# Performance work log

Hardware: AMD Instinct MI355X
Metric: run time of the kernel (lower is better)

The kernel has to match this reference:

```python
import jax, jax.numpy as jnp
import numpy as np
import math

L, D, H, HD, F, G, V, P = 15, 512, 64, 8, 2048, 128, 7, 49
B, N = 4, 256


def setup_inputs() -> dict:
    key = jax.random.key(0)
    ks = jax.random.split(key, 24)
    nrm = lambda k, shape, s=0.02: (jax.random.normal(k, shape) * s).astype(jnp.float32)
    inp = {}
    inp["atom_types"] = jax.random.randint(ks[0], (B, N), 0, V)
    inp["coords"] = jax.random.normal(ks[1], (B, N, 3)) * 3.0
    inp["pair_types"] = jax.random.randint(ks[2], (B, N, N), 0, P)
    inp["mask"] = jnp.ones((B, N), dtype=bool)
    # embeddings / pair encoding params
    inp["atom_emb"] = nrm(ks[3], (V, D), 1.0).at[0].set(0.0)  # padding_idx=0
    inp["gaussian_mu"] = jax.random.normal(ks[4], (G,))
    inp["gaussian_sigma"] = jnp.ones((G,)) * 0.1
    inp["pair_a"] = jax.random.normal(ks[5], (P,)) * 0.01
    inp["pair_b"] = jax.random.normal(ks[6], (P,)) * 0.01
    inp["pl_w"] = nrm(ks[7], (G,))
    inp["pl_b"] = jnp.zeros(())
    # stacked per-layer params (leading dim L for lax.scan)
    inp["ln1_g"] = jnp.ones((L, D)); inp["ln1_b"] = jnp.zeros((L, D))
    inp["qkv_w"] = nrm(ks[8], (L, 3 * D, D)); inp["qkv_b"] = jnp.zeros((L, 3 * D))
    inp["pp_w"] = nrm(ks[9], (L, H), 0.1); inp["pp_b"] = jnp.zeros((L, H))
    inp["out_w"] = nrm(ks[10], (L, D, D)); inp["out_b"] = jnp.zeros((L, D))
    inp["ln2_g"] = jnp.ones((L, D)); inp["ln2_b"] = jnp.zeros((L, D))
    inp["ffn_w1"] = nrm(ks[11], (L, F, D)); inp["ffn_b1"] = jnp.zeros((L, F))
    inp["ffn_w2"] = nrm(ks[12], (L, D, F)); inp["ffn_b2"] = jnp.zeros((L, D))
    # SE3 head scalar affines (Linear(1,1) twice) and energy head
    inp["se3_uw"] = jnp.array(0.5); inp["se3_ub"] = jnp.array(0.01)
    inp["se3_ww"] = jnp.array(0.5); inp["se3_wb"] = jnp.array(0.01)
    inp["en_w"] = nrm(ks[13], (D,)); inp["en_b"] = jnp.zeros(())
    return inp


def _layernorm(x, g, b):
    m = x.mean(-1, keepdims=True)
    v = ((x - m) ** 2).mean(-1, keepdims=True)
    return (x - m) / jnp.sqrt(v + 1e-5) * g + b


def reference(atom_types, coords, pair_types, mask,
              atom_emb, gaussian_mu, gaussian_sigma, pair_a, pair_b, pl_w, pl_b,
              ln1_g, ln1_b, qkv_w, qkv_b, pp_w, pp_b, out_w, out_b,
              ln2_g, ln2_b, ffn_w1, ffn_b1, ffn_w2, ffn_b2,
              se3_uw, se3_ub, se3_ww, se3_wb, en_w, en_b):
    b_, n_ = atom_types.shape
    h = atom_emb[atom_types]  # [B,N,D]

    delta = coords[:, :, None, :] - coords[:, None, :, :]  # [B,N,N,3]
    d2 = (delta ** 2).sum(-1)
    dist = jnp.sqrt(jnp.maximum(d2, 1e-12))  # safe norm (grad-safe at 0)
    dist = jnp.where(mask[:, :, None], dist, 0.0)
    da = (pair_a[pair_types] * dist + pair_b[pair_types])[..., None]  # [B,N,N,1]
    gt = jnp.exp(-(da - gaussian_mu) ** 2) / (2.0 * gaussian_sigma ** 2)
    gt = gt / (gaussian_sigma * math.sqrt(2.0 * math.pi))
    gt = gt * mask[:, :, None, None]  # [B,N,N,G]
    pair_repr = gt @ pl_w + pl_b  # [B,N,N]
    pair_mask = mask[:, :, None] & mask[:, None, :]
    pair_repr = pair_repr * pair_mask

    scale = 1.0 / math.sqrt(HD)
    row_mask = mask[:, None, :, None]  # masks query rows, per original code

    def layer(hc, p):
        (l1g, l1b, qw, qb, ppw, ppb, ow, ob, l2g, l2b, w1, b1, w2, b2) = p
        x = _layernorm(hc, l1g, l1b)
        qkv = (x @ qw.T + qb).reshape(b_, n_, 3, H, HD)
        q, k, v = qkv[:, :, 0], qkv[:, :, 1], qkv[:, :, 2]
        scores = jnp.einsum('bnhd,bmhd->bhnm', q, k) * scale
        bias = pair_repr[..., None] * ppw + ppb  # [B,N,N,H]
        scores = scores + bias.transpose(0, 3, 1, 2)
        scores = jnp.where(row_mask, scores, -1e9)
        probs = jax.nn.softmax(scores, axis=-1)
        probs = jnp.where(jnp.isnan(probs), 0.0, probs)
        attn = jnp.einsum('bhnm,bmhd->bnhd', probs, v).reshape(b_, n_, D)
        hc = hc + attn @ ow.T + ob
        x2 = _layernorm(hc, l2g, l2b)
        ffn = jax.nn.gelu(x2 @ w1.T + b1, approximate=False) @ w2.T + b2
        return hc + ffn, None

    h, _ = jax.lax.scan(layer, h, (ln1_g, ln1_b, qkv_w, qkv_b, pp_w, pp_b,
                                   out_w, out_b, ln2_g, ln2_b,
                                   ffn_w1, ffn_b1, ffn_w2, ffn_b2))

    # --- SE3 equivariant head ---
    c = jax.nn.relu(pair_repr)[..., None]  # [B,N,N,1]
    c = c * se3_uw + se3_ub
    c = c * se3_ww + se3_wb
    c = c * mask[:, :, None, None]
    update = (delta * c).sum(axis=2)  # [B,N,3]
    num_valid = mask.sum(-1).astype(coords.dtype)[:, None, None] + 1e-6
    pred_coords = coords + update / num_valid

    cls = h[:, 0, :]
    pred_energy = cls @ en_w + en_b  # [B]
    return pred_coords, pred_energy


if __name__ == '__main__':
    out = reference(**setup_inputs())
    print(out[0].shape, out[1].shape)
```

## Files before the change

kernel.cpp:

```cpp
#include <hip/hip_runtime.h>
#include <hip/hip_bf16.h>
#include <math.h>

#define LAY 15
#define DIM 512
#define NH 64
#define HD 8
#define FF 2048
#define NG 128
#define BATCH 4
#define NTOK 256
#define PSTRIDE 524288

typedef __attribute__((ext_vector_type(8))) short short8;
typedef __attribute__((ext_vector_type(4))) short short4v;
typedef __attribute__((ext_vector_type(2))) short short2v;
typedef __attribute__((ext_vector_type(8))) __bf16 bf16x8;
typedef __attribute__((ext_vector_type(4))) float f32x4;

__device__ inline short f2bs(float f) {
  __bf16 b = (__bf16)f;
  return __builtin_bit_cast(short, b);
}

__global__ __launch_bounds__(256) void embed_kernel(
    const int* __restrict__ types, const float* __restrict__ emb,
    float* __restrict__ h)
{
  int idx = blockIdx.x * 256 + threadIdx.x;
  int token = idx >> 9;
  int d = idx & 511;
  h[idx] = emb[types[token] * DIM + d];
}

__global__ __launch_bounds__(256) void cvt2_kernel(
    const float* __restrict__ qkvw, const float* __restrict__ outw,
    const float* __restrict__ w1, const float* __restrict__ w2,
    short* __restrict__ dst, int basePair)
{
  size_t i = ((size_t)basePair + blockIdx.x * 256 + threadIdx.x) * 2;
  const float* src; size_t off;
  if (i < 1474560)      { src = qkvw; off = i; }
  else if (i < 1966080) { src = outw; off = i - 1474560; }
  else if (i < 3932160) { src = w1;   off = i - 1966080; }
  else                  { src = w2;   off = i - 3932160; }
  const float4* sp = (const float4*)(src + off * 8);
  float4 a = sp[0], b = sp[1], c = sp[2], d = sp[3];
  bf16x8 v0, v1;
  v0[0] = (__bf16)a.x; v0[1] = (__bf16)a.y; v0[2] = (__bf16)a.z; v0[3] = (__bf16)a.w;
  v0[4] = (__bf16)b.x; v0[5] = (__bf16)b.y; v0[6] = (__bf16)b.z; v0[7] = (__bf16)b.w;
  v1[0] = (__bf16)c.x; v1[1] = (__bf16)c.y; v1[2] = (__bf16)c.z; v1[3] = (__bf16)c.w;
  v1[4] = (__bf16)d.x; v1[5] = (__bf16)d.y; v1[6] = (__bf16)d.z; v1[7] = (__bf16)d.w;
  *(short8*)(dst + i * 8) = __builtin_bit_cast(short8, v0);
  *(short8*)(dst + i * 8 + 8) = __builtin_bit_cast(short8, v1);
}

__global__ __launch_bounds__(256) void pair_kernel(
    const int* __restrict__ pair_types, const float* __restrict__ coords,
    const float* __restrict__ mu, const float* __restrict__ sigma,
    const float* __restrict__ pa, const float* __restrict__ pb,
    const float* __restrict__ plw, const float* __restrict__ plb,
    const float* __restrict__ uw, const float* __restrict__ ub,
    const float* __restrict__ ww, const float* __restrict__ wb,
    float* __restrict__ pair_repr, float* __restrict__ out)
{
  __shared__ float smu[NG], sw[NG];
  __shared__ float sm[4][3];
  int tid = threadIdx.x;
  if (tid < NG) {
    float sg = sigma[tid];
    smu[tid] = mu[tid];
    sw[tid] = plw[tid] / (2.0f * sg * sg * sg * 2.5066282746310002f);
  }
  __syncthreads();
  int bi = blockIdx.x;
  int b = bi >> 8;
  int j = tid;
  int idx = bi * 256 + j;
  const float* ci = coords + bi * 3;
  const float* cj = coords + (b * NTOK + j) * 3;
  float dx = ci[0] - cj[0], dy = ci[1] - cj[1], dz = ci[2] - cj[2];
  float d2 = dx * dx + dy * dy + dz * dz;
  float dist = sqrtf(fmaxf(d2, 1e-12f));
  int pt = pair_types[idx];
  float da = pa[pt] * dist + pb[pt];
  float acc = 0.0f;
#pragma unroll 8
  for (int g = 0; g < NG; ++g) {
    float t = da - smu[g];
    acc += __expf(-t * t) * sw[g];
  }
  float pr = acc + plb[0];
  pair_repr[idx] = pr;

  float c = fmaxf(pr, 0.0f);
  c = c * uw[0] + ub[0];
  c = c * ww[0] + wb[0];
  float sx = dx * c, sy = dy * c, sz = dz * c;
#pragma unroll
  for (int o = 32; o > 0; o >>= 1) {
    sx += __shfl_xor(sx, o);
    sy += __shfl_xor(sy, o);
    sz += __shfl_xor(sz, o);
  }
  if ((j & 63) == 0) {
    sm[j >> 6][0] = sx; sm[j >> 6][1] = sy; sm[j >> 6][2] = sz;
  }
  __syncthreads();
  if (j < 3) {
    float u = sm[0][j] + sm[1][j] + sm[2][j] + sm[3][j];
    out[bi * 3 + j] = coords[bi * 3 + j] + u * (1.0f / (256.0f + 1e-6f));
  }
}

__global__ __launch_bounds__(256) void pairT_kernel(
    const float* __restrict__ pr, float* __restrict__ prT)
{
  __shared__ float tile[32][33];
  int b = blockIdx.z;
  int i0 = blockIdx.y * 32, j0 = blockIdx.x * 32;
  int tx = threadIdx.x & 31, ty = threadIdx.x >> 5;
#pragma unroll
  for (int r = 0; r < 4; ++r)
    tile[ty + r * 8][tx] = pr[((size_t)(b * NTOK + i0 + ty + r * 8)) * NTOK + j0 + tx];
  __syncthreads();
#pragma unroll
  for (int r = 0; r < 4; ++r)
    prT[((size_t)(b * NTOK + j0 + ty + r * 8)) * NTOK + i0 + tx] = tile[tx][ty + r * 8];
}

__global__ __launch_bounds__(256) void ln_kernel(
    const float* __restrict__ h, const float* __restrict__ g,
    const float* __restrict__ beta, short* __restrict__ x)
{
  int t = blockIdx.x;
  int tid = threadIdx.x;
  float2 v = *(const float2*)&h[(size_t)t * DIM + tid * 2];
  __shared__ float sm[4];
  float s = v.x + v.y;
#pragma unroll
  for (int o = 32; o > 0; o >>= 1) s += __shfl_xor(s, o);
  if ((tid & 63) == 0) sm[tid >> 6] = s;
  __syncthreads();
  float mean = (sm[0] + sm[1] + sm[2] + sm[3]) * (1.0f / 512.0f);
  float d0 = v.x - mean, d1 = v.y - mean;
  float ss = d0 * d0 + d1 * d1;
#pragma unroll
  for (int o = 32; o > 0; o >>= 1) ss += __shfl_xor(ss, o);
  __syncthreads();
  if ((tid & 63) == 0) sm[tid >> 6] = ss;
  __syncthreads();
  float var = (sm[0] + sm[1] + sm[2] + sm[3]) * (1.0f / 512.0f);
  float rstd = rsqrtf(var + 1e-5f);
  float2 gg = *(const float2*)&g[tid * 2];
  float2 bb = *(const float2*)&beta[tid * 2];
  short2v o2;
  o2[0] = f2bs(d0 * rstd * gg.x + bb.x);
  o2[1] = f2bs(d1 * rstd * gg.y + bb.y);
  *(short2v*)&x[(size_t)t * DIM + tid * 2] = o2;
}

__global__ __launch_bounds__(256) void ln_res_kernel(
    float* __restrict__ h, const float* __restrict__ part, int kparts,
    const float* __restrict__ g, const float* __restrict__ beta,
    short* __restrict__ x)
{
  int t = blockIdx.x;
  int tid = threadIdx.x;
  size_t base = (size_t)t * DIM + tid * 2;
  float2 v = *(const float2*)&h[base];
  for (int z = 0; z < kparts; ++z) {
    float2 pz = *(const float2*)&part[(size_t)z * PSTRIDE + base];
    v.x += pz.x; v.y += pz.y;
  }
  *(float2*)&h[base] = v;
  __shared__ float sm[4];
  float s = v.x + v.y;
#pragma unroll
  for (int o = 32; o > 0; o >>= 1) s += __shfl_xor(s, o);
  if ((tid & 63) == 0) sm[tid >> 6] = s;
  __syncthreads();
  float mean = (sm[0] + sm[1] + sm[2] + sm[3]) * (1.0f / 512.0f);
  float d0 = v.x - mean, d1 = v.y - mean;
  float ss = d0 * d0 + d1 * d1;
#pragma unroll
  for (int o = 32; o > 0; o >>= 1) ss += __shfl_xor(ss, o);
  __syncthreads();
  if ((tid & 63) == 0) sm[tid >> 6] = ss;
  __syncthreads();
  float var = (sm[0] + sm[1] + sm[2] + sm[3]) * (1.0f / 512.0f);
  float rstd = rsqrtf(var + 1e-5f);
  float2 gg = *(const float2*)&g[tid * 2];
  float2 bb = *(const float2*)&beta[tid * 2];
  short2v o2;
  o2[0] = f2bs(d0 * rstd * gg.x + bb.x);
  o2[1] = f2bs(d1 * rstd * gg.y + bb.y);
  *(short2v*)&x[base] = o2;
}

template <int MODE>
__global__ __launch_bounds__(128) void mm3(
    const short* __restrict__ A, const short* __restrict__ W,
    const float* __restrict__ bias, float* __restrict__ Cf,
    short* __restrict__ Cb, int N, int K, int kparts)
{
  __shared__ short As[2][2048];
  __shared__ short Bs[2][8192];
  int tid = threadIdx.x;
  int lane = tid & 63, wv = tid >> 6;
  int fr = lane & 15, fq = lane >> 4;
  int m0 = blockIdx.y * 32, n0 = blockIdx.x * 128;
  int Ksub = K / kparts;
  int kbeg = blockIdx.z * Ksub, kend = kbeg + Ksub;

  int arow[2], acol[2], brow[8], bcol[8];
#pragma unroll
  for (int r = 0; r < 2; ++r) {
    int id = r * 128 + tid;
    arow[r] = id >> 3;
    acol[r] = (id & 7) ^ (arow[r] & 7);
  }
#pragma unroll
  for (int r = 0; r < 8; ++r) {
    int id = r * 128 + tid;
    brow[r] = id >> 3;
    bcol[r] = (id & 7) ^ (brow[r] & 7);
  }

  auto stage = [&](int p, int k0) {
#pragma unroll
    for (int r = 0; r < 2; ++r) {
      const short* ga = &A[(size_t)(m0 + arow[r]) * K + k0 + acol[r] * 8];
      __builtin_amdgcn_global_load_lds(
          (const __attribute__((address_space(1))) void*)ga,
          (__attribute__((address_space(3))) void*)&As[p][(r * 128 + wv * 64) * 8],
          16, 0, 0);
    }
#pragma unroll
    for (int r = 0; r < 8; ++r) {
      const short* gw = &W[(size_t)(n0 + brow[r]) * K + k0 + bcol[r] * 8];
      __builtin_amdgcn_global_load_lds(
          (const __attribute__((address_space(1))) void*)gw,
          (__attribute__((address_space(3))) void*)&Bs[p][(r * 128 + wv * 64) * 8],
          16, 0, 0);
    }
  };

  f32x4 acc[2][4];
#pragma unroll
  for (int i = 0; i < 2; ++i)
#pragma unroll
    for (int j = 0; j < 4; ++j) acc[i][j] = (f32x4){0.f, 0.f, 0.f, 0.f};

  int aslot[2][2], bslot[2][4];
#pragma unroll
  for (int s = 0; s < 2; ++s) {
    int c = s * 4 + fq;
#pragma unroll
    for (int i = 0; i < 2; ++i) {
      int m = i * 16 + fr;
      aslot[s][i] = m * 8 + (c ^ (m & 7));
    }
#pragma unroll
    for (int j = 0; j < 4; ++j) {
      int n = wv * 64 + j * 16 + fr;
      bslot[s][j] = n * 8 + (c ^ (n & 7));
    }
  }

  stage(0, kbeg);
  __syncthreads();
  int p = 0;
  for (int k0 = kbeg; k0 < kend; k0 += 64) {
    if (k0 + 64 < kend) stage(p ^ 1, k0 + 64);
    short8 af[2][2], bf_[2][4];
#pragma unroll
    for (int s = 0; s < 2; ++s) {
#pragma unroll
      for (int i = 0; i < 2; ++i)
        af[s][i] = *(const short8*)&As[p][aslot[s][i] * 8];
#pragma unroll
      for (int j = 0; j < 4; ++j)
        bf_[s][j] = *(const short8*)&Bs[p][bslot[s][j] * 8];
    }
#pragma unroll
    for (int s = 0; s < 2; ++s)
#pragma unroll
      for (int i = 0; i < 2; ++i)
#pragma unroll
        for (int j = 0; j < 4; ++j)
          acc[i][j] = __builtin_amdgcn_mfma_f32_16x16x32_bf16(
              af[s][i], bf_[s][j], acc[i][j], 0, 0, 0);
    __syncthreads();
    p ^= 1;
  }

#pragma unroll
  for (int i = 0; i < 2; ++i) {
#pragma unroll
    for (int j = 0; j < 4; ++j) {
      int col = n0 + wv * 64 + j * 16 + fr;
      float bcol = bias[col];
#pragma unroll
      for (int rr = 0; rr < 4; ++rr) {
        int row = m0 + i * 16 + fq * 4 + rr;
        size_t idx = (size_t)row * N + col;
        float v = acc[i][j][rr];
        if (MODE == 2) {
          v += bcol;
          Cb[idx] = f2bs(0.5f * v * (1.0f + erff(v * 0.70710678118654752f)));
        } else if (MODE == 3) {
          Cb[idx] = f2bs(v + bcol);
        } else {
          if (blockIdx.z == 0) v += bcol;
          Cf[(size_t)blockIdx.z * PSTRIDE + idx] = v;
        }
      }
    }
  }
}

__global__ __launch_bounds__(128) void attn_mfma(
    const short* __restrict__ qkv, const float* __restrict__ prT,
    const float* __restrict__ ppw, const float* __restrict__ ppb,
    short* __restrict__ attn)
{
  __shared__ alignas(16) short Kl[256 * 8];
  __shared__ alignas(16) short Ql[128 * 8];
  __shared__ alignas(16) short VT[8 * 264];
  __shared__ alignas(16) short P[2 * 16 * 264];
  __shared__ alignas(16) float linv[32];
  int h = blockIdx.x, b = blockIdx.y;
  int qbase = blockIdx.z * 128;
  int tid = threadIdx.x;

#pragma unroll
  for (int r0 = 0; r0 < 2; ++r0) {
    int r = tid + r0 * 128;
    short8 kv = *(const short8*)&qkv[(size_t)(b * NTOK + r) * 1536 + 512 + h * 8];
    *(short8*)&Kl[r * 8] = kv;
    short8 vv = *(const short8*)&qkv[(size_t)(b * NTOK + r) * 1536 + 1024 + h * 8];
#pragma unroll
    for (int d = 0; d < 8; ++d) VT[d * 264 + r] = vv[d];
  }
  {
    short8 qv = *(const short8*)&qkv[(size_t)(b * NTOK + qbase + tid) * 1536 + h * 8];
    *(short8*)&Ql[tid * 8] = qv;
  }
  __syncthreads();

  int lane = tid & 63, w = tid >> 6;
  int fr = lane & 15, quad = lane >> 4;
  float pw = ppw[h], pbb = ppb[h];
  const float scale = 0.35355339059327373f;
  short8 zero8 = {0, 0, 0, 0, 0, 0, 0, 0};

  short8 vfrag[8];
#pragma unroll
  for (int kc = 0; kc < 8; ++kc)
    vfrag[kc] = (fr < 8) ? *(const short8*)&VT[fr * 264 + kc * 32 + quad * 8]
                         : zero8;

  short* Pw = &P[w * 16 * 264];
  float* lw = &linv[w * 16];

  for (int qt = 0; qt < 4; ++qt) {
    int qloc = w * 64 + qt * 16;
    int qg = qbase + qloc + fr;
    const float* prp = &prT[(size_t)b * 65536 + qg];
    float prv[16][4];
#pragma unroll
    for (int t = 0; t < 16; ++t)
#pragma unroll
      for (int r = 0; r < 4; ++r)
        prv[t][r] = prp[(size_t)(t * 16 + quad * 4 + r) * NTOK];

    short8 qf = zero8;
    if (quad == 0) qf = *(const short8*)&Ql[(qloc + fr) * 8];
    f32x4 sacc[16];
#pragma unroll
    for (int t = 0; t < 16; ++t) {
      short8 kf = zero8;
      if (quad == 0) kf = *(const short8*)&Kl[(t * 16 + fr) * 8];
      sacc[t] = __builtin_amdgcn_mfma_f32_16x16x32_bf16(
          kf, qf, (f32x4){0.f, 0.f, 0.f, 0.f}, 0, 0, 0);
    }

    float l = 0.f;
#pragma unroll
    for (int t = 0; t < 16; ++t) {
      short4v pk;
#pragma unroll
      for (int r = 0; r < 4; ++r) {
        float s = sacc[t][r] * scale + prv[t][r] * pw + pbb;
        float p = __expf(s);
        l += p;
        pk[r] = f2bs(p);
      }
      *(short4v*)&Pw[fr * 264 + t * 16 + quad * 4] = pk;
    }
    l += __shfl_xor(l, 16);
    l += __shfl_xor(l, 32);
    if (lane < 16) lw[fr] = 1.0f / l;

    f32x4 oacc = (f32x4){0.f, 0.f, 0.f, 0.f};
#pragma unroll
    for (int kc = 0; kc < 8; ++kc) {
      short8 pf = *(const short8*)&Pw[fr * 264 + kc * 32 + quad * 8];
      oacc = __builtin_amdgcn_mfma_f32_16x16x32_bf16(pf, vfrag[kc], oacc, 0, 0, 0);
    }
    if (fr < 8) {
      f32x4 li = *(f32x4*)&lw[quad * 4];
#pragma unroll
      for (int r = 0; r < 4; ++r) {
        int q = qbase + qloc + quad * 4 + r;
        attn[(size_t)(b * NTOK + q) * DIM + h * 8 + fr] = f2bs(oacc[r] * li[r]);
      }
    }
  }
}

__global__ __launch_bounds__(256) void energy_kernel(
    const float* __restrict__ h, const float* __restrict__ part,
    const float* __restrict__ enw, const float* __restrict__ enb,
    float* __restrict__ out)
{
  int b = blockIdx.x;
  int tid = threadIdx.x;
  size_t base = (size_t)(b * NTOK) * DIM;
  float x0 = h[base + tid], x1 = h[base + tid + 256];
#pragma unroll
  for (int z = 0; z < 4; ++z) {
    x0 += part[(size_t)z * PSTRIDE + base + tid];
    x1 += part[(size_t)z * PSTRIDE + base + tid + 256];
  }
  float s = x0 * enw[tid] + x1 * enw[tid + 256];
  __shared__ float sm[4];
#pragma unroll
  for (int o = 32; o > 0; o >>= 1) s += __shfl_xor(s, o);
  if ((tid & 63) == 0) sm[tid >> 6] = s;
  __syncthreads();
  if (tid == 0) out[BATCH * NTOK * 3 + b] = sm[0] + sm[1] + sm[2] + sm[3] + enb[0];
}

extern "C" void kernel_launch(void* const* d_in, const int* in_sizes, int n_in,
                              void* d_out, int out_size, void* d_ws, size_t ws_size,
                              hipStream_t stream)
{
  const int*   atom_types = (const int*)d_in[0];
  const float* coords     = (const float*)d_in[1];
  const int*   pair_types = (const int*)d_in[2];
  const float* atom_emb = (const float*)d_in[4];
  const float* gmu  = (const float*)d_in[5];
  const float* gsig = (const float*)d_in[6];
  const float* pa   = (const float*)d_in[7];
  const float* pb   = (const float*)d_in[8];
  const float* plw  = (const float*)d_in[9];
  const float* plb  = (const float*)d_in[10];
  const float* ln1g = (const float*)d_in[11];
  const float* ln1b = (const float*)d_in[12];
  const float* qkvw = (const float*)d_in[13];
  const float* qkvb = (const float*)d_in[14];
  const float* ppw  = (const float*)d_in[15];
  const float* ppb  = (const float*)d_in[16];
  const float* outw = (const float*)d_in[17];
  const float* outb = (const float*)d_in[18];
  const float* ln2g = (const float*)d_in[19];
  const float* ln2b = (const float*)d_in[20];
  const float* w1   = (const float*)d_in[21];
  const float* b1   = (const float*)d_in[22];
  const float* w2   = (const float*)d_in[23];
  const float* b2   = (const float*)d_in[24];
  const float* uw   = (const float*)d_in[25];
  const float* ub   = (const float*)d_in[26];
  const float* sww  = (const float*)d_in[27];
  const float* swb  = (const float*)d_in[28];
  const float* enw  = (const float*)d_in[29];
  const float* enb  = (const float*)d_in[30];

  float* out = (float*)d_out;
  float* ws  = (float*)d_ws;
  float* pair_repr = ws;
  float* prT  = pair_repr + 262144;
  float* h    = prT + 262144;
  float* part = h + 524288;
  short* qkv_bf  = (short*)(part + 4 * 524288);
  short* x_bf    = qkv_bf + 1572864;
  short* attn_bf = x_bf + 524288;
  short* ffn1_bf = attn_bf + 524288;
  short* qkvw_bf = ffn1_bf + 2097152;
  short* outw_bf = qkvw_bf + 11796480;
  short* w1_bf   = outw_bf + 3932160;
  short* w2_bf   = w1_bf + 15728640;

  cvt2_kernel<<<11520, 256, 0, stream>>>(qkvw, outw, w1, w2, qkvw_bf, 0);

  embed_kernel<<<2048, 256, 0, stream>>>(atom_types, atom_emb, h);
  pair_kernel<<<1024, 256, 0, stream>>>(pair_types, coords, gmu, gsig, pa, pb,
                                        plw, plb, uw, ub, sww, swb,
                                        pair_repr, out);
  pairT_kernel<<<dim3(8, 8, 4), 256, 0, stream>>>(pair_repr, prT);

  for (int l = 0; l < LAY; ++l) {
    if (l == 0)
      ln_kernel<<<1024, 256, 0, stream>>>(h, ln1g, ln1b, x_bf);
    else
      ln_res_kernel<<<1024, 256, 0, stream>>>(h, part, 4,
                                              ln1g + l * DIM, ln1b + l * DIM, x_bf);
    mm3<3><<<dim3(12, 32, 1), 128, 0, stream>>>(
        x_bf, qkvw_bf + (size_t)l * 1536 * DIM, qkvb + l * 1536, nullptr, qkv_bf,
        1536, DIM, 1);
    attn_mfma<<<dim3(NH, BATCH, 2), 128, 0, stream>>>(
        qkv_bf, prT, ppw + l * NH, ppb + l * NH, attn_bf);
    mm3<4><<<dim3(4, 32, 2), 128, 0, stream>>>(
        attn_bf, outw_bf + (size_t)l * DIM * DIM, outb + l * DIM, part, nullptr,
        DIM, DIM, 2);
    ln_res_kernel<<<1024, 256, 0, stream>>>(h, part, 2,
                                            ln2g + l * DIM, ln2b + l * DIM, x_bf);
    mm3<2><<<dim3(16, 32, 1), 128, 0, stream>>>(
        x_bf, w1_bf + (size_t)l * FF * DIM, b1 + l * FF, nullptr, ffn1_bf,
        FF, DIM, 1);
    mm3<4><<<dim3(4, 32, 4), 128, 0, stream>>>(
        ffn1_bf, w2_bf + (size_t)l * DIM * FF, b2 + l * DIM, part, nullptr,
        DIM, FF, 4);
  }
  energy_kernel<<<BATCH, 256, 0, stream>>>(h, part, enw, enb, out);
}
```

Baseline: 1.246 ms.

## Shrink GEMM tiles to single-wave 32x32 with triple-buffered async loads

Each GEMM block becomes one wave computing a 32x32 tile instead of two waves computing 32x128. The K loop is fully unrolled with a 3-stage LDS ring, using explicit vmcnt waits instead of __syncthreads so prefetches overlap the MFMAs. This quadruples the block count to fill more CUs, at the cost of more redundant A-tile loads and less reuse per block. The weight conversion kernel is also simplified to convert four floats per thread.

```diff
diff --git a/kernel.cpp b/kernel.cpp
--- a/kernel.cpp
+++ b/kernel.cpp
@@ -33,26 +33,21 @@
   h[idx] = emb[types[token] * DIM + d];
 }
 
-__global__ __launch_bounds__(256) void cvt2_kernel(
+__global__ __launch_bounds__(256) void cvt_kernel(
     const float* __restrict__ qkvw, const float* __restrict__ outw,
     const float* __restrict__ w1, const float* __restrict__ w2,
-    short* __restrict__ dst, int basePair)
-{
-  size_t i = ((size_t)basePair + blockIdx.x * 256 + threadIdx.x) * 2;
-  const float* src; size_t off;
-  if (i < 1474560)      { src = qkvw; off = i; }
-  else if (i < 1966080) { src = outw; off = i - 1474560; }
-  else if (i < 3932160) { src = w1;   off = i - 1966080; }
-  else                  { src = w2;   off = i - 3932160; }
-  const float4* sp = (const float4*)(src + off * 8);
-  float4 a = sp[0], b = sp[1], c = sp[2], d = sp[3];
-  bf16x8 v0, v1;
-  v0[0] = (__bf16)a.x; v0[1] = (__bf16)a.y; v0[2] = (__bf16)a.z; v0[3] = (__bf16)a.w;
-  v0[4] = (__bf16)b.x; v0[5] = (__bf16)b.y; v0[6] = (__bf16)b.z; v0[7] = (__bf16)b.w;
-  v1[0] = (__bf16)c.x; v1[1] = (__bf16)c.y; v1[2] = (__bf16)c.z; v1[3] = (__bf16)c.w;
-  v1[4] = (__bf16)d.x; v1[5] = (__bf16)d.y; v1[6] = (__bf16)d.z; v1[7] = (__bf16)d.w;
-  *(short8*)(dst + i * 8) = __builtin_bit_cast(short8, v0);
-  *(short8*)(dst + i * 8 + 8) = __builtin_bit_cast(short8, v1);
+    short* __restrict__ dst)
+{
+  int i = blockIdx.x * 256 + threadIdx.x;
+  const float* src; int off;
+  if (i < 2949120)      { src = qkvw; off = i; }
+  else if (i < 3932160) { src = outw; off = i - 2949120; }
+  else if (i < 7864320) { src = w1;   off = i - 3932160; }
+  else                  { src = w2;   off = i - 7864320; }
+  float4 f = ((const float4*)src)[off];
+  short4v o;
+  o[0] = f2bs(f.x); o[1] = f2bs(f.y); o[2] = f2bs(f.z); o[3] = f2bs(f.w);
+  *(short4v*)(dst + (size_t)i * 4) = o;
 }
 
 __global__ __launch_bounds__(256) void pair_kernel(
@@ -198,61 +193,51 @@
   *(short2v*)&x[base] = o2;
 }
 
-template <int MODE>
-__global__ __launch_bounds__(128) void mm3(
+template <int MODE, int TSTEPS>
+__global__ __launch_bounds__(64) void mm3(
     const short* __restrict__ A, const short* __restrict__ W,
     const float* __restrict__ bias, float* __restrict__ Cf,
-    short* __restrict__ Cb, int N, int K, int kparts)
-{
-  __shared__ short As[2][2048];
-  __shared__ short Bs[2][8192];
+    short* __restrict__ Cb, int N, int K)
+{
+  __shared__ alignas(16) short As[3][2048];
+  __shared__ alignas(16) short Bs[3][2048];
   int tid = threadIdx.x;
-  int lane = tid & 63, wv = tid >> 6;
-  int fr = lane & 15, fq = lane >> 4;
-  int m0 = blockIdx.y * 32, n0 = blockIdx.x * 128;
-  int Ksub = K / kparts;
-  int kbeg = blockIdx.z * Ksub, kend = kbeg + Ksub;
-
-  int arow[2], acol[2], brow[8], bcol[8];
-#pragma unroll
-  for (int r = 0; r < 2; ++r) {
-    int id = r * 128 + tid;
-    arow[r] = id >> 3;
-    acol[r] = (id & 7) ^ (arow[r] & 7);
-  }
-#pragma unroll
-  for (int r = 0; r < 8; ++r) {
-    int id = r * 128 + tid;
-    brow[r] = id >> 3;
-    bcol[r] = (id & 7) ^ (brow[r] & 7);
-  }
+  int fr = tid & 15, fq = (tid >> 4) & 3;
+  int m0 = blockIdx.y * 32, n0 = blockIdx.x * 32;
+  int kbeg = blockIdx.z * (TSTEPS * 64);
 
   auto stage = [&](int p, int k0) {
 #pragma unroll
-    for (int r = 0; r < 2; ++r) {
-      const short* ga = &A[(size_t)(m0 + arow[r]) * K + k0 + acol[r] * 8];
+    for (int r = 0; r < 4; ++r) {
+      int id = r * 64 + tid;
+      int row = id >> 3;
+      int col = (id & 7) ^ (row & 7);
+      const short* ga = &A[(size_t)(m0 + row) * K + k0 + col * 8];
       __builtin_amdgcn_global_load_lds(
           (const __attribute__((address_space(1))) void*)ga,
-          (__attribute__((address_space(3))) void*)&As[p][(r * 128 + wv * 64) * 8],
+          (__attribute__((address_space(3))) void*)&As[p][r * 512],
           16, 0, 0);
     }
 #pragma unroll
-    for (int r = 0; r < 8; ++r) {
-      const short* gw = &W[(size_t)(n0 + brow[r]) * K + k0 + bcol[r] * 8];
+    for (int r = 0; r < 4; ++r) {
+      int id = r * 64 + tid;
+      int row = id >> 3;
+      int col = (id & 7) ^ (row & 7);
+      const short* gw = &W[(size_t)(n0 + row) * K + k0 + col * 8];
       __builtin_amdgcn_global_load_lds(
           (const __attribute__((address_space(1))) void*)gw,
-          (__attribute__((address_space(3))) void*)&Bs[p][(r * 128 + wv * 64) * 8],
+          (__attribute__((address_space(3))) void*)&Bs[p][r * 512],
           16, 0, 0);
     }
   };
 
-  f32x4 acc[2][4];
+  f32x4 acc[2][2];
 #pragma unroll
   for (int i = 0; i < 2; ++i)
 #pragma unroll
-    for (int j = 0; j < 4; ++j) acc[i][j] = (f32x4){0.f, 0.f, 0.f, 0.f};
-
-  int aslot[2][2], bslot[2][4];
+    for (int j = 0; j < 2; ++j) acc[i][j] = (f32x4){0.f, 0.f, 0.f, 0.f};
+
+  int aslot[2][2], bslot[2][2];
 #pragma unroll
   for (int s = 0; s < 2; ++s) {
     int c = s * 4 + fq;
@@ -260,46 +245,46 @@
     for (int i = 0; i < 2; ++i) {
       int m = i * 16 + fr;
       aslot[s][i] = m * 8 + (c ^ (m & 7));
-    }
-#pragma unroll
-    for (int j = 0; j < 4; ++j) {
-      int n = wv * 64 + j * 16 + fr;
-      bslot[s][j] = n * 8 + (c ^ (n & 7));
+      bslot[s][i] = m * 8 + (c ^ (m & 7));
     }
   }
 
   stage(0, kbeg);
-  __syncthreads();
-  int p = 0;
-  for (int k0 = kbeg; k0 < kend; k0 += 64) {
-    if (k0 + 64 < kend) stage(p ^ 1, k0 + 64);
-    short8 af[2][2], bf_[2][4];
-#pragma unroll
-    for (int s = 0; s < 2; ++s) {
+  stage(1, kbeg + 64);
+  stage(2, kbeg + 128);
+
+#pragma unroll
+  for (int t = 0; t < TSTEPS; ++t) {
+    if (t < TSTEPS - 2)       asm volatile("s_waitcnt vmcnt(16)" ::: "memory");
+    else if (t == TSTEPS - 2) asm volatile("s_waitcnt vmcnt(8)" ::: "memory");
+    else                      asm volatile("s_waitcnt vmcnt(0)" ::: "memory");
+    int p = t % 3;
+    short8 af[2][2], bf_[2][2];
+#pragma unroll
+    for (int s = 0; s < 2; ++s)
+#pragma unroll
+      for (int i = 0; i < 2; ++i) {
+        af[s][i]  = *(const short8*)&As[p][aslot[s][i] * 8];
+        bf_[s][i] = *(const short8*)&Bs[p][bslot[s][i] * 8];
+      }
+    asm volatile("s_waitcnt lgkmcnt(0)" ::: "memory");
+    __builtin_amdgcn_sched_barrier(0);
+    if (t + 3 < TSTEPS) stage(p, kbeg + (t + 3) * 64);
+#pragma unroll
+    for (int s = 0; s < 2; ++s)
 #pragma unroll
       for (int i = 0; i < 2; ++i)
-        af[s][i] = *(const short8*)&As[p][aslot[s][i] * 8];
-#pragma unroll
-      for (int j = 0; j < 4; ++j)
-        bf_[s][j] = *(const short8*)&Bs[p][bslot[s][j] * 8];
-    }
-#pragma unroll
-    for (int s = 0; s < 2; ++s)
-#pragma unroll
-      for (int i = 0; i < 2; ++i)
-#pragma unroll
-        for (int j = 0; j < 4; ++j)
+#pragma unroll
+        for (int j = 0; j < 2; ++j)
           acc[i][j] = __builtin_amdgcn_mfma_f32_16x16x32_bf16(
               af[s][i], bf_[s][j], acc[i][j], 0, 0, 0);
-    __syncthreads();
-    p ^= 1;
   }
 
 #pragma unroll
   for (int i = 0; i < 2; ++i) {
 #pragma unroll
-    for (int j = 0; j < 4; ++j) {
-      int col = n0 + wv * 64 + j * 16 + fr;
+    for (int j = 0; j < 2; ++j) {
+      int col = n0 + j * 16 + fr;
       float bcol = bias[col];
 #pragma unroll
       for (int rr = 0; rr < 4; ++rr) {
@@ -493,7 +478,7 @@
   short* w1_bf   = outw_bf + 3932160;
   short* w2_bf   = w1_bf + 15728640;
 
-  cvt2_kernel<<<11520, 256, 0, stream>>>(qkvw, outw, w1, w2, qkvw_bf, 0);
+  cvt_kernel<<<46080, 256, 0, stream>>>(qkvw, outw, w1, w2, qkvw_bf);
 
   embed_kernel<<<2048, 256, 0, stream>>>(atom_types, atom_emb, h);
   pair_kernel<<<1024, 256, 0, stream>>>(pair_types, coords, gmu, gsig, pa, pb,
@@ -507,22 +492,22 @@
     else
       ln_res_kernel<<<1024, 256, 0, stream>>>(h, part, 4,
                                               ln1g + l * DIM, ln1b + l * DIM, x_bf);
-    mm3<3><<<dim3(12, 32, 1), 128, 0, stream>>>(
+    mm3<3, 8><<<dim3(48, 32, 1), 64, 0, stream>>>(
         x_bf, qkvw_bf + (size_t)l * 1536 * DIM, qkvb + l * 1536, nullptr, qkv_bf,
-        1536, DIM, 1);
+        1536, DIM);
     attn_mfma<<<dim3(NH, BATCH, 2), 128, 0, stream>>>(
         qkv_bf, prT, ppw + l * NH, ppb + l * NH, attn_bf);
-    mm3<4><<<dim3(4, 32, 2), 128, 0, stream>>>(
+    mm3<4, 4><<<dim3(16, 32, 2), 64, 0, stream>>>(
         attn_bf, outw_bf + (size_t)l * DIM * DIM, outb + l * DIM, part, nullptr,
-        DIM, DIM, 2);
+        DIM, DIM);
     ln_res_kernel<<<1024, 256, 0, stream>>>(h, part, 2,
                                             ln2g + l * DIM, ln2b + l * DIM, x_bf);
-    mm3<2><<<dim3(16, 32, 1), 128, 0, stream>>>(
+    mm3<2, 8><<<dim3(64, 32, 1), 64, 0, stream>>>(
         x_bf, w1_bf + (size_t)l * FF * DIM, b1 + l * FF, nullptr, ffn1_bf,
-        FF, DIM, 1);
-    mm3<4><<<dim3(4, 32, 4), 128, 0, stream>>>(
+        FF, DIM);
+    mm3<4, 8><<<dim3(16, 32, 4), 64, 0, stream>>>(
         ffn1_bf, w2_bf + (size_t)l * DIM * FF, b2 + l * DIM, part, nullptr,
-        DIM, FF, 4);
+        DIM, FF);
   }
   energy_kernel<<<BATCH, 256, 0, stream>>>(h, part, enw, enb, out);
 }
```

New measurement: 1.142 ms. -8.4%, faster.
